# Kernel optimization log

Hardware: AMD Instinct MI355X
Metric: run time of the kernel (lower is better)

The kernel has to match this reference:

```python
import jax, jax.numpy as jnp
import numpy as np

SCALE = 1.0

def setup_inputs() -> dict:
    key = jax.random.key(0)
    k1, k2, k3 = jax.random.split(key, 3)
    N, K, H, W = 4, 8, 512, 512
    C, P = 16, 1000000
    fragments = jax.random.randint(k1, (N, K, H, W), 0, P, dtype=jnp.int32)
    zbuf = jax.random.uniform(k2, (N, K, H, W), dtype=jnp.float32)
    ptclds = jax.random.normal(k3, (C, P), dtype=jnp.float32)
    return {"fragments": fragments, "zbuf": zbuf, "ptclds": ptclds}

def reference(fragments, zbuf, ptclds):
    # zbuf < 0 means no point assigned; replace with -1e-4 as in original
    z = jnp.where(zbuf < 0, jnp.float32(-0.0001), zbuf)
    importance = 1.0 / (z + 1e-06)                      # (N, K, H, W)
    weights = jax.nn.softmax(importance * SCALE, axis=1)  # softmax over K
    # gather point features: (C, N, K, H, W)
    gathered = ptclds[:, fragments]
    # weighted sum over K -> (N, C, H, W)
    images = jnp.einsum('nkhw,cnkhw->nchw', weights, gathered)
    return images
```

## Files before the change

kernel.cpp:

```cpp
#include <hip/hip_runtime.h>

#define NN 4
#define KK 8
#define HH 512
#define WW 512
#define CC 16
#define PP 1000000

__global__ __launch_bounds__(256) void transpose_tbl(
    const float* __restrict__ ptclds, float* __restrict__ tbl) {
  int p = blockIdx.x * blockDim.x + threadIdx.x;
  if (p >= PP) return;
  float v[CC];
#pragma unroll
  for (int c = 0; c < CC; ++c) v[c] = ptclds[(size_t)c * PP + p];
  float4* o = reinterpret_cast<float4*>(tbl + (size_t)p * CC);
  o[0] = make_float4(v[0], v[1], v[2], v[3]);
  o[1] = make_float4(v[4], v[5], v[6], v[7]);
  o[2] = make_float4(v[8], v[9], v[10], v[11]);
  o[3] = make_float4(v[12], v[13], v[14], v[15]);
}

template <int TRANSPOSED>
__global__ __launch_bounds__(256) void composite(
    const int* __restrict__ frag, const float* __restrict__ zbuf,
    const float* __restrict__ tbl, float* __restrict__ out) {
  const int HW = HH * WW;
  int g = blockIdx.x * blockDim.x + threadIdx.x;
  if (g >= NN * HW) return;
  int n = g / HW;
  int hw = g - n * HW;

  const int* fp = frag + (size_t)n * KK * HW + hw;
  const float* zp = zbuf + (size_t)n * KK * HW + hw;

  float imp[KK];
  int idx[KK];
  float m = -3.402823e38f;
#pragma unroll
  for (int k = 0; k < KK; ++k) {
    float z = zp[(size_t)k * HW];
    idx[k] = fp[(size_t)k * HW];
    z = (z < 0.0f) ? -0.0001f : z;
    float im = 1.0f / (z + 1e-6f);
    imp[k] = im;
    m = fmaxf(m, im);
  }
  float e[KK];
  float s = 0.0f;
#pragma unroll
  for (int k = 0; k < KK; ++k) {
    e[k] = __expf(imp[k] - m);
    s += e[k];
  }
  float rs = 1.0f / s;

  float acc[CC];
#pragma unroll
  for (int c = 0; c < CC; ++c) acc[c] = 0.0f;

#pragma unroll
  for (int k = 0; k < KK; ++k) {
    float wk = e[k] * rs;
    if (TRANSPOSED) {
      const float4* tp = reinterpret_cast<const float4*>(tbl + (size_t)idx[k] * CC);
      float4 a = tp[0], b = tp[1], c4 = tp[2], d = tp[3];
      acc[0]  += wk * a.x;  acc[1]  += wk * a.y;
      acc[2]  += wk * a.z;  acc[3]  += wk * a.w;
      acc[4]  += wk * b.x;  acc[5]  += wk * b.y;
      acc[6]  += wk * b.z;  acc[7]  += wk * b.w;
      acc[8]  += wk * c4.x; acc[9]  += wk * c4.y;
      acc[10] += wk * c4.z; acc[11] += wk * c4.w;
      acc[12] += wk * d.x;  acc[13] += wk * d.y;
      acc[14] += wk * d.z;  acc[15] += wk * d.w;
    } else {
#pragma unroll
      for (int c = 0; c < CC; ++c)
        acc[c] += wk * tbl[(size_t)c * PP + idx[k]];
    }
  }

  float* op = out + (size_t)n * CC * HW + hw;
#pragma unroll
  for (int c = 0; c < CC; ++c) op[(size_t)c * HW] = acc[c];
}

extern "C" void kernel_launch(void* const* d_in, const int* in_sizes, int n_in,
                              void* d_out, int out_size, void* d_ws, size_t ws_size,
                              hipStream_t stream) {
  const int* frag = (const int*)d_in[0];
  const float* zbuf = (const float*)d_in[1];
  const float* ptclds = (const float*)d_in[2];
  float* out = (float*)d_out;

  const int HW = HH * WW;
  const int npix = NN * HW;
  const size_t tbl_bytes = (size_t)PP * CC * sizeof(float);

  if (ws_size >= tbl_bytes) {
    float* tbl = (float*)d_ws;
    transpose_tbl<<<(PP + 255) / 256, 256, 0, stream>>>(ptclds, tbl);
    composite<1><<<(npix + 255) / 256, 256, 0, stream>>>(frag, zbuf, tbl, out);
  } else {
    composite<0><<<(npix + 255) / 256, 256, 0, stream>>>(frag, zbuf, ptclds, out);
  }
}
```

Baseline: 330.7 us.

## Transpose point table through LDS and batch gather loads in composite

The transpose kernel now stages 64 points by 16 channels in padded shared memory, so both the reads and the float4 writes are coalesced. Before this, each thread wrote 64 contiguous bytes, which strided badly across the wavefront. The composite kernel issues all four table gathers for a group of four fragments before accumulating, which raises memory-level parallelism. It also moves the softmax normalisation to a single multiply at the output and replaces 64-bit index math and division with shifts. The cost is higher register pressure from the 16 in-flight float4 loads, and the grid size PP/64 assumes P divides by 64.

```diff
diff --git a/kernel.cpp b/kernel.cpp
--- a/kernel.cpp
+++ b/kernel.cpp
@@ -9,16 +9,21 @@
 
 __global__ __launch_bounds__(256) void transpose_tbl(
     const float* __restrict__ ptclds, float* __restrict__ tbl) {
-  int p = blockIdx.x * blockDim.x + threadIdx.x;
-  if (p >= PP) return;
-  float v[CC];
+  __shared__ float lds[64][17];
+  const int base = blockIdx.x * 64;
+  const int p  = threadIdx.x & 63;
+  const int c0 = (threadIdx.x >> 6) * 4;
 #pragma unroll
-  for (int c = 0; c < CC; ++c) v[c] = ptclds[(size_t)c * PP + p];
-  float4* o = reinterpret_cast<float4*>(tbl + (size_t)p * CC);
-  o[0] = make_float4(v[0], v[1], v[2], v[3]);
-  o[1] = make_float4(v[4], v[5], v[6], v[7]);
-  o[2] = make_float4(v[8], v[9], v[10], v[11]);
-  o[3] = make_float4(v[12], v[13], v[14], v[15]);
+  for (int i = 0; i < 4; ++i) {
+    int c = c0 + i;
+    lds[p][c] = ptclds[(size_t)c * PP + base + p];
+  }
+  __syncthreads();
+  const int po = threadIdx.x >> 2;
+  const int q  = threadIdx.x & 3;
+  float4 v = make_float4(lds[po][q * 4 + 0], lds[po][q * 4 + 1],
+                         lds[po][q * 4 + 2], lds[po][q * 4 + 3]);
+  reinterpret_cast<float4*>(tbl)[(size_t)blockIdx.x * 256 + threadIdx.x] = v;
 }
 
 template <int TRANSPOSED>
@@ -28,29 +33,28 @@
   const int HW = HH * WW;
   int g = blockIdx.x * blockDim.x + threadIdx.x;
   if (g >= NN * HW) return;
-  int n = g / HW;
-  int hw = g - n * HW;
+  int n = g >> 18;
+  int hw = g & (HW - 1);
 
   const int* fp = frag + (size_t)n * KK * HW + hw;
   const float* zp = zbuf + (size_t)n * KK * HW + hw;
 
-  float imp[KK];
   int idx[KK];
+  float e[KK];
   float m = -3.402823e38f;
 #pragma unroll
   for (int k = 0; k < KK; ++k) {
-    float z = zp[(size_t)k * HW];
-    idx[k] = fp[(size_t)k * HW];
+    float z = zp[k * HW];
+    idx[k] = fp[k * HW];
     z = (z < 0.0f) ? -0.0001f : z;
     float im = 1.0f / (z + 1e-6f);
-    imp[k] = im;
+    e[k] = im;
     m = fmaxf(m, im);
   }
-  float e[KK];
   float s = 0.0f;
 #pragma unroll
   for (int k = 0; k < KK; ++k) {
-    e[k] = __expf(imp[k] - m);
+    e[k] = __expf(e[k] - m);
     s += e[k];
   }
   float rs = 1.0f / s;
@@ -59,30 +63,41 @@
 #pragma unroll
   for (int c = 0; c < CC; ++c) acc[c] = 0.0f;
 
+  if (TRANSPOSED) {
 #pragma unroll
-  for (int k = 0; k < KK; ++k) {
-    float wk = e[k] * rs;
-    if (TRANSPOSED) {
-      const float4* tp = reinterpret_cast<const float4*>(tbl + (size_t)idx[k] * CC);
-      float4 a = tp[0], b = tp[1], c4 = tp[2], d = tp[3];
-      acc[0]  += wk * a.x;  acc[1]  += wk * a.y;
-      acc[2]  += wk * a.z;  acc[3]  += wk * a.w;
-      acc[4]  += wk * b.x;  acc[5]  += wk * b.y;
-      acc[6]  += wk * b.z;  acc[7]  += wk * b.w;
-      acc[8]  += wk * c4.x; acc[9]  += wk * c4.y;
-      acc[10] += wk * c4.z; acc[11] += wk * c4.w;
-      acc[12] += wk * d.x;  acc[13] += wk * d.y;
-      acc[14] += wk * d.z;  acc[15] += wk * d.w;
-    } else {
+    for (int kb = 0; kb < 2; ++kb) {
+      float4 q0[4], q1[4], q2[4], q3[4];
+#pragma unroll
+      for (int j = 0; j < 4; ++j) {
+        const float4* tp =
+            reinterpret_cast<const float4*>(tbl + (size_t)idx[kb * 4 + j] * CC);
+        q0[j] = tp[0]; q1[j] = tp[1]; q2[j] = tp[2]; q3[j] = tp[3];
+      }
+#pragma unroll
+      for (int j = 0; j < 4; ++j) {
+        float wk = e[kb * 4 + j];
+        acc[0]  += wk * q0[j].x;  acc[1]  += wk * q0[j].y;
+        acc[2]  += wk * q0[j].z;  acc[3]  += wk * q0[j].w;
+        acc[4]  += wk * q1[j].x;  acc[5]  += wk * q1[j].y;
+        acc[6]  += wk * q1[j].z;  acc[7]  += wk * q1[j].w;
+        acc[8]  += wk * q2[j].x;  acc[9]  += wk * q2[j].y;
+        acc[10] += wk * q2[j].z;  acc[11] += wk * q2[j].w;
+        acc[12] += wk * q3[j].x;  acc[13] += wk * q3[j].y;
+        acc[14] += wk * q3[j].z;  acc[15] += wk * q3[j].w;
+      }
+    }
+  } else {
+#pragma unroll
+    for (int k = 0; k < KK; ++k) {
 #pragma unroll
       for (int c = 0; c < CC; ++c)
-        acc[c] += wk * tbl[(size_t)c * PP + idx[k]];
+        acc[c] += e[k] * tbl[(size_t)c * PP + idx[k]];
     }
   }
 
   float* op = out + (size_t)n * CC * HW + hw;
 #pragma unroll
-  for (int c = 0; c < CC; ++c) op[(size_t)c * HW] = acc[c];
+  for (int c = 0; c < CC; ++c) op[c * HW] = acc[c] * rs;
 }
 
 extern "C" void kernel_launch(void* const* d_in, const int* in_sizes, int n_in,
@@ -99,7 +114,7 @@
 
   if (ws_size >= tbl_bytes) {
     float* tbl = (float*)d_ws;
-    transpose_tbl<<<(PP + 255) / 256, 256, 0, stream>>>(ptclds, tbl);
+    transpose_tbl<<<PP / 64, 256, 0, stream>>>(ptclds, tbl);
     composite<1><<<(npix + 255) / 256, 256, 0, stream>>>(frag, zbuf, tbl, out);
   } else {
     composite<0><<<(npix + 255) / 256, 256, 0, stream>>>(frag, zbuf, ptclds, out);
```

Measured after the change: 322.4 us. 2.5% less time.
